# Kernel optimization log

Hardware: AMD Instinct MI355X
Metric: run time of the kernel (lower is better)

Reference implementation:

```python
import math
import jax, jax.numpy as jnp
import numpy as np

NUM_HEADS = 12
HEAD_DIM = 64
HIDDEN = NUM_HEADS * HEAD_DIM  # 768
SEQ = 4096


def setup_inputs() -> dict:
    key = jax.random.key(0)
    ks = jax.random.split(key, 7)
    s = 0.02  # BERT-style init scale for weights
    return {
        "hidden_states": jax.random.normal(ks[0], (1, SEQ, HIDDEN), jnp.float32),
        "Wq": jax.random.normal(ks[1], (HIDDEN, HIDDEN), jnp.float32) * s,
        "bq": jax.random.normal(ks[2], (HIDDEN,), jnp.float32) * s,
        "Wk": jax.random.normal(ks[3], (HIDDEN, HIDDEN), jnp.float32) * s,
        "bk": jax.random.normal(ks[4], (HIDDEN,), jnp.float32) * s,
        "Wv": jax.random.normal(ks[5], (HIDDEN, HIDDEN), jnp.float32) * s,
        "bv": jax.random.normal(ks[6], (HIDDEN,), jnp.float32) * s,
    }


def _split_heads(z):
    # [S, HIDDEN] -> [H, S, dh]
    S = z.shape[0]
    return jnp.transpose(z.reshape(S, NUM_HEADS, HEAD_DIM), (1, 0, 2))


def reference(hidden_states, Wq, bq, Wk, bk, Wv, bv):
    # batch is squeezed in the original module (kernel is unbatched)
    x = hidden_states[0]  # [S, D]
    q = _split_heads(x @ Wq.T + bq)  # [H, S, dh]
    k = _split_heads(x @ Wk.T + bk)  # [H, S, dh]
    scale = 1.0 / math.sqrt(HEAD_DIM)
    scores = jnp.einsum('hqd,hkd->hqk', q, k) * scale  # [H, S, S]
    probs = jax.nn.softmax(scores, axis=-1)
    # multi_rand_attn_cuda approximates P @ (x @ Wv^T + bv) via CDF-driven
    # Monte-Carlo column sampling of Wv; its expectation is the exact product,
    # which is the correctness baseline computed here.
    v = _split_heads(x @ Wv.T + bv)  # [H, S, dh]
    ctx = jnp.einsum('hqk,hkd->hqd', probs, v)  # [H, S, dh]
    ctx = jnp.transpose(ctx, (1, 0, 2)).reshape(x.shape[0], HIDDEN)
    return ctx[None]  # [1, S, D]
```

## Files before the change

kernel.cpp:

```cpp
#include <hip/hip_runtime.h>
#include <stdint.h>


typedef float    f32x4 __attribute__((ext_vector_type(4)));
typedef _Float16 h16x8 __attribute__((ext_vector_type(8)));
typedef _Float16 h16x4 __attribute__((ext_vector_type(4)));
typedef _Float16 h16x2 __attribute__((ext_vector_type(2)));
typedef __fp16   fp16x2 __attribute__((ext_vector_type(2)));
typedef unsigned short u16;

#define MFMA32(A, B, C) __builtin_amdgcn_mfma_f32_16x16x32_f16((A), (B), (C), 0, 0, 0)
#define ZERO4 ((f32x4){0.f, 0.f, 0.f, 0.f})

#define SEQ 4096
#define HID 768
#define NH  12
#define DH  64

#define CEXP 0.18033688011112042f

#define WAITV(N) asm volatile("s_waitcnt vmcnt(" #N ")" ::: "memory")
#define SBAR()   __builtin_amdgcn_s_barrier()
#define SCHED0() __builtin_amdgcn_sched_barrier(0)

__device__ __forceinline__ u16 f2h(float f) {
  union { _Float16 h; u16 u; } v;
  v.h = (_Float16)f;
  return v.u;
}
__device__ __forceinline__ float h2f(u16 u) {
  union { u16 u; _Float16 h; } v;
  v.u = u;
  return (float)v.h;
}

__device__ __forceinline__ void gload_lds16(const void* g, void* l) {
  __builtin_amdgcn_global_load_lds(
      (__attribute__((address_space(1))) void*)(g),
      (__attribute__((address_space(3))) void*)(l),
      16, 0, 0);
}

__global__ __launch_bounds__(256) void cast_all_k(
    const float* __restrict__ x,  const float* __restrict__ wq,
    const float* __restrict__ wk, const float* __restrict__ wv,
    u16* __restrict__ xh,  u16* __restrict__ wqh,
    u16* __restrict__ wkh, u16* __restrict__ wvh)
{
  int i = blockIdx.x * 256 + threadIdx.x;
  const int NX4 = (SEQ * HID) / 4;
  const int NW4 = (HID * HID) / 4;
  const float4* src; ushort4* dst; int idx;
  if (i < NX4) {
    src = (const float4*)x; dst = (ushort4*)xh; idx = i;
  } else {
    int j = i - NX4;
    int w = j / NW4;
    idx = j - w * NW4;
    src = (const float4*)(w == 0 ? wq : (w == 1 ? wk : wv));
    dst = (ushort4*)(w == 0 ? wqh : (w == 1 ? wkh : wvh));
  }
  float4 v = src[idx];
  ushort4 o;
  o.x = f2h(v.x); o.y = f2h(v.y); o.z = f2h(v.z); o.w = f2h(v.w);
  dst[idx] = o;
}

__global__ __launch_bounds__(256, 3) void qkv_gemm_k(
    const u16* __restrict__ xh,
    const u16* __restrict__ wqh, const u16* __restrict__ wkh, const u16* __restrict__ wvh,
    const float* __restrict__ bq, const float* __restrict__ bk, const float* __restrict__ bv,
    u16* __restrict__ Qh, u16* __restrict__ Kh, u16* __restrict__ Vt)
{
  __shared__ u16 S[128 * 128];

  const int t = threadIdx.x;
  const int wave = t >> 6, lane = t & 63;
  const int m = lane & 15, quad = lane >> 4;
  const int z  = blockIdx.z;
  const int n0 = blockIdx.x * 128;
  const int m0 = blockIdx.y * 128;

  const u16*   W    = (z == 0) ? wqh : (z == 1) ? wkh : wvh;
  const float* bias = (z == 0) ? bq  : (z == 1) ? bk  : bv;

  const int wm = (wave >> 1) * 64;
  const int wn = (wave & 1) * 64;

  f32x4 acc[4][4];
#pragma unroll
  for (int i = 0; i < 4; i++)
#pragma unroll
    for (int j = 0; j < 4; j++) acc[i][j] = ZERO4;

  const int srow = wave * 8 + (lane >> 3);
  const int scg  = (lane & 7) ^ (srow & 7);
  const u16* gA = xh + (m0 + srow) * HID + scg * 8;
  const u16* gB = W  + (n0 + srow) * HID + scg * 8;
  u16* lA = S + wave * 512;
  u16* lB = S + 8192 + wave * 512;

  for (int k0 = 0; k0 < HID; k0 += 64) {
    __syncthreads();
#pragma unroll
    for (int c = 0; c < 4; c++) {
      gload_lds16(gA + c * 32 * HID + k0, lA + c * 2048);
      gload_lds16(gB + c * 32 * HID + k0, lB + c * 2048);
    }
    __syncthreads();

#pragma unroll
    for (int s = 0; s < 2; s++) {
      h16x8 af[4], bf[4];
#pragma unroll
      for (int i = 0; i < 4; i++)
        af[i] = *(const h16x8*)(S + (wm + i * 16 + m) * 64
                                + ((s * 4 + quad) ^ (m & 7)) * 8);
#pragma unroll
      for (int j = 0; j < 4; j++)
        bf[j] = *(const h16x8*)(S + 8192 + (wn + j * 16 + m) * 64
                                + ((s * 4 + quad) ^ (m & 7)) * 8);
#pragma unroll
      for (int i = 0; i < 4; i++)
#pragma unroll
        for (int j = 0; j < 4; j++)
          acc[i][j] = MFMA32(af[i], bf[j], acc[i][j]);
    }
  }

  __syncthreads();

  if (z < 2) {
    const float sc = (z == 0) ? CEXP : 1.0f;
#pragma unroll
    for (int i = 0; i < 4; i++) {
      int sl = wm + i * 16 + quad * 4;
#pragma unroll
      for (int j = 0; j < 4; j++) {
        int colp = wn + j * 16 + m;
        float bb = bias[n0 + colp];
        int c = colp >> 3, sub = colp & 7;
#pragma unroll
        for (int r = 0; r < 4; r++)
          S[(sl + r) * 128 + ((c ^ ((sl + r) & 15)) * 8) + sub] =
              f2h((acc[i][j][r] + bb) * sc);
      }
    }
    __syncthreads();
    u16* outp = (z == 0) ? Qh : Kh;
    const int ch = t & 15;
#pragma unroll
    for (int rr = 0; rr < 8; rr++) {
      int s = rr * 16 + (t >> 4);
      h16x8 v = *(const h16x8*)(S + s * 128 + ((ch ^ (s & 15)) * 8));
      *(h16x8*)(outp + (m0 + s) * HID + n0 + ch * 8) = v;
    }
  } else {
#pragma unroll
    for (int i = 0; i < 4; i++) {
      int sl = wm + i * 16 + quad * 4;
      int vp = (sl & ~31) + ((sl >> 2) & 3) * 8 + ((sl >> 4) & 1) * 4;
#pragma unroll
      for (int j = 0; j < 4; j++) {
        int nl = wn + j * 16 + m;
        float bb = bias[n0 + nl];
        h16x4 o;
        o[0] = (_Float16)(acc[i][j][0] + bb);
        o[1] = (_Float16)(acc[i][j][1] + bb);
        o[2] = (_Float16)(acc[i][j][2] + bb);
        o[3] = (_Float16)(acc[i][j][3] + bb);
        *(h16x4*)(S + nl * 128 + (((vp >> 3) ^ (nl & 15)) * 8) + (vp & 7)) = o;
      }
    }
    __syncthreads();
    const int ch = t & 15;
#pragma unroll
    for (int rr = 0; rr < 8; rr++) {
      int n = rr * 16 + (t >> 4);
      h16x8 v = *(const h16x8*)(S + n * 128 + ((ch ^ (n & 15)) * 8));
      *(h16x8*)(Vt + (n0 + n) * SEQ + m0 + ch * 8) = v;
    }
  }
}


__device__ __forceinline__ void stage_kv(const u16* gKb, const u16* gVb,
                                         u16* lK, u16* lV, int kv0)
{
#pragma unroll
  for (int c = 0; c < 2; c++) {
    gload_lds16(gKb + (kv0 + c * 32) * HID, lK + c * 2048);
    gload_lds16(gVb + c * 32 * SEQ + kv0,   lV + c * 2048);
  }
}

__device__ __forceinline__ void attn_compute(
    const u16* __restrict__ Kb, const u16* __restrict__ Vb,
    const h16x8 (&qf)[2][2], f32x4 (&O)[2][4], f32x4 (&Lacc)[2],
    h16x8 onesv, int m, int quad)
{
#pragma unroll
  for (int p = 0; p < 2; ++p) {
    const int krow0 = 32 * p + m;
    const int krow1 = krow0 + 16;
    h16x8 kb00 = *(const h16x8*)(Kb + krow0 * 64 + ((    quad) ^ (m & 7)) * 8);
    h16x8 kb01 = *(const h16x8*)(Kb + krow0 * 64 + ((4 + quad) ^ (m & 7)) * 8);
    h16x8 kb10 = *(const h16x8*)(Kb + krow1 * 64 + ((    quad) ^ (m & 7)) * 8);
    h16x8 kb11 = *(const h16x8*)(Kb + krow1 * 64 + ((4 + quad) ^ (m & 7)) * 8);

    h16x8 vb[4];
#pragma unroll
    for (int jd = 0; jd < 4; jd++) {
      int d = jd * 16 + m;
      vb[jd] = *(const h16x8*)(Vb + d * 64 + (((p * 4 + quad) ^ (m & 7)) * 8));
    }

#pragma unroll
    for (int qn = 0; qn < 2; qn++) {
      __builtin_amdgcn_s_setprio(1);
      f32x4 S0 = MFMA32(kb00, qf[qn][0], ZERO4);
      S0       = MFMA32(kb01, qf[qn][1], S0);
      f32x4 S1 = MFMA32(kb10, qf[qn][0], ZERO4);
      S1       = MFMA32(kb11, qf[qn][1], S1);
      __builtin_amdgcn_s_setprio(0);

      float e0 = __builtin_amdgcn_exp2f(S0[0]);
      float e1 = __builtin_amdgcn_exp2f(S0[1]);
      float e2 = __builtin_amdgcn_exp2f(S0[2]);
      float e3 = __builtin_amdgcn_exp2f(S0[3]);
      float e4 = __builtin_amdgcn_exp2f(S1[0]);
      float e5 = __builtin_amdgcn_exp2f(S1[1]);
      float e6 = __builtin_amdgcn_exp2f(S1[2]);
      float e7 = __builtin_amdgcn_exp2f(S1[3]);

      fp16x2 p01 = __builtin_amdgcn_cvt_pkrtz(e0, e1);
      fp16x2 p23 = __builtin_amdgcn_cvt_pkrtz(e2, e3);
      fp16x2 p45 = __builtin_amdgcn_cvt_pkrtz(e4, e5);
      fp16x2 p67 = __builtin_amdgcn_cvt_pkrtz(e6, e7);
      h16x2 q01 = __builtin_bit_cast(h16x2, p01);
      h16x2 q23 = __builtin_bit_cast(h16x2, p23);
      h16x2 q45 = __builtin_bit_cast(h16x2, p45);
      h16x2 q67 = __builtin_bit_cast(h16x2, p67);
      h16x4 pl = __builtin_shufflevector(q01, q23, 0, 1, 2, 3);
      h16x4 ph = __builtin_shufflevector(q45, q67, 0, 1, 2, 3);
      h16x8 pa = __builtin_shufflevector(pl, ph, 0, 1, 2, 3, 4, 5, 6, 7);

      __builtin_amdgcn_s_setprio(1);
#pragma unroll
      for (int jd = 0; jd < 4; jd++)
        O[qn][jd] = MFMA32(pa, vb[jd], O[qn][jd]);
      Lacc[qn] = MFMA32(pa, onesv, Lacc[qn]);
      __builtin_amdgcn_s_setprio(0);
    }
  }
}

__global__ __launch_bounds__(256, 3) void attn_k(
    const u16* __restrict__ Qh, const u16* __restrict__ Kh, const u16* __restrict__ Vt,
    float* __restrict__ out0, u16* __restrict__ Op1, float* __restrict__ Lp)
{
  __shared__ u16 Ks[3][64 * 64];
  __shared__ u16 Vs[3][64 * 64];

  const int t = threadIdx.x;
  const int wave = t >> 6, lane = t & 63;
  const int m = lane & 15, quad = lane >> 4;
  const int h  = blockIdx.y;
  const int q0 = blockIdx.x * 128;
  const int sp = blockIdx.z;
  const int kvbase = sp * 2048;

  h16x8 qf[2][2];
#pragma unroll
  for (int qn = 0; qn < 2; qn++)
#pragma unroll
    for (int ks = 0; ks < 2; ks++)
      qf[qn][ks] = *(const h16x8*)(Qh + (q0 + wave * 32 + qn * 16 + m) * HID
                                   + h * DH + ks * 32 + quad * 8);

  f32x4 O[2][4];
#pragma unroll
  for (int qn = 0; qn < 2; qn++)
#pragma unroll
    for (int jd = 0; jd < 4; jd++) O[qn][jd] = ZERO4;
  f32x4 Lacc[2] = {ZERO4, ZERO4};

  h16x8 onesv;
#pragma unroll
  for (int j = 0; j < 8; j++) onesv[j] = (_Float16)1.0f;

  const int srow = wave * 8 + (lane >> 3);
  const int swz  = ((lane & 7) ^ (srow & 7)) * 8;
  const u16* gKb = Kh + srow * HID + h * DH + swz;
  const u16* gVb = Vt + (h * DH + srow) * SEQ + swz;
  u16* lK0 = &Ks[0][wave * 512]; u16* lV0 = &Vs[0][wave * 512];
  u16* lK1 = &Ks[1][wave * 512]; u16* lV1 = &Vs[1][wave * 512];
  u16* lK2 = &Ks[2][wave * 512]; u16* lV2 = &Vs[2][wave * 512];

  stage_kv(gKb, gVb, lK0, lV0, kvbase);
  stage_kv(gKb, gVb, lK1, lV1, kvbase + 64);

  for (int it = 0; it < 30; it += 3) {
    WAITV(4); SBAR(); SCHED0();
    stage_kv(gKb, gVb, lK2, lV2, kvbase + (it + 2) * 64);
    attn_compute(&Ks[0][0], &Vs[0][0], qf, O, Lacc, onesv, m, quad);
    SCHED0();

    WAITV(4); SBAR(); SCHED0();
    stage_kv(gKb, gVb, lK0, lV0, kvbase + (it + 3) * 64);
    attn_compute(&Ks[1][0], &Vs[1][0], qf, O, Lacc, onesv, m, quad);
    SCHED0();

    WAITV(4); SBAR(); SCHED0();
    stage_kv(gKb, gVb, lK1, lV1, kvbase + (it + 4) * 64);
    attn_compute(&Ks[2][0], &Vs[2][0], qf, O, Lacc, onesv, m, quad);
    SCHED0();
  }
  WAITV(4); SBAR(); SCHED0();
  attn_compute(&Ks[0][0], &Vs[0][0], qf, O, Lacc, onesv, m, quad);
  SCHED0();
  WAITV(0); SBAR(); SCHED0();
  attn_compute(&Ks[1][0], &Vs[1][0], qf, O, Lacc, onesv, m, quad);

#pragma unroll
  for (int qn = 0; qn < 2; qn++) {
    if (m == 0) {
#pragma unroll
      for (int r = 0; r < 4; r++)
        Lp[sp * NH * SEQ + h * SEQ + q0 + wave * 32 + qn * 16 + quad * 4 + r] =
            Lacc[qn][r];
    }
#pragma unroll
    for (int jd = 0; jd < 4; jd++) {
      int col = h * DH + jd * 16 + m;
#pragma unroll
      for (int r = 0; r < 4; r++) {
        int row = q0 + wave * 32 + qn * 16 + quad * 4 + r;
        if (sp == 0) out0[row * HID + col] = O[qn][jd][r];
        else         Op1[row * HID + col] = f2h(O[qn][jd][r]);
      }
    }
  }
}

__global__ __launch_bounds__(256) void reduce_k(
    float* __restrict__ out, const u16* __restrict__ Op1,
    const float* __restrict__ Lp)
{
  int i = blockIdx.x * 256 + threadIdx.x;
  int s  = i / 192;
  int c4 = i - s * 192;
  int h  = c4 >> 4;
  float L = Lp[h * SEQ + s] + Lp[NH * SEQ + h * SEQ + s];
  float inv = __builtin_amdgcn_rcpf(L);
  float4 a = ((const float4*)out)[i];
  ushort4 b = ((const ushort4*)Op1)[i];
  float4 r;
  r.x = (a.x + h2f(b.x)) * inv;
  r.y = (a.y + h2f(b.y)) * inv;
  r.z = (a.z + h2f(b.z)) * inv;
  r.w = (a.w + h2f(b.w)) * inv;
  ((float4*)out)[i] = r;
}

extern "C" void kernel_launch(void* const* d_in, const int* in_sizes, int n_in,
                              void* d_out, int out_size, void* d_ws, size_t ws_size,
                              hipStream_t stream) {
  const float* x  = (const float*)d_in[0];
  const float* Wq = (const float*)d_in[1];
  const float* bq = (const float*)d_in[2];
  const float* Wk = (const float*)d_in[3];
  const float* bk = (const float*)d_in[4];
  const float* Wv = (const float*)d_in[5];
  const float* bv = (const float*)d_in[6];
  float* out = (float*)d_out;

  char* ws = (char*)d_ws;
  u16* Qh  = (u16*)(ws);
  u16* Kh  = (u16*)(ws + 6291456);
  u16* Vt  = (u16*)(ws + 12582912);
  u16* xh  = (u16*)(ws + 18874368);
  u16* wqh = (u16*)(ws + 25165824);
  u16* wkh = (u16*)(ws + 26345472);
  u16* wvh = (u16*)(ws + 27525120);
  u16*   Op1 = (u16*)(ws + 18874368);
  float* Lp  = (float*)(ws + 25165824);

  cast_all_k<<<4800, 256, 0, stream>>>(x, Wq, Wk, Wv, xh, wqh, wkh, wvh);
  qkv_gemm_k<<<dim3(6, 32, 3), 256, 0, stream>>>(xh, wqh, wkh, wvh,
                                                 bq, bk, bv, Qh, Kh, Vt);
  attn_k<<<dim3(32, NH, 2), 256, 0, stream>>>(Qh, Kh, Vt, out, Op1, Lp);
  reduce_k<<<3072, 256, 0, stream>>>(out, Op1, Lp);
}
```

Measured before the change: 158.1 us.

## Load K tiles directly into double-buffered registers instead of staging in LDS

K tiles for the attention loop are now read straight from global memory into two alternating register banks, one tile ahead of use. V alone is staged through LDS, now in a four-slot ring. The wait counts are rewritten to match the new load order. This removes the LDS round trip and LDS traffic for K, but every wave now fetches the full K tile itself, which multiplies K global/L2 reads, and it adds 64 VGPRs of register pressure under a 3-block occupancy bound.

```diff
diff --git a/kernel.cpp b/kernel.cpp
--- a/kernel.cpp
+++ b/kernel.cpp
@@ -184,30 +184,34 @@
 }
 
 
-__device__ __forceinline__ void stage_kv(const u16* gKb, const u16* gVb,
-                                         u16* lK, u16* lV, int kv0)
-{
-#pragma unroll
-  for (int c = 0; c < 2; c++) {
-    gload_lds16(gKb + (kv0 + c * 32) * HID, lK + c * 2048);
-    gload_lds16(gVb + c * 32 * SEQ + kv0,   lV + c * 2048);
-  }
+__device__ __forceinline__ void stage_v(const u16* gVb, u16* lV, int kv0)
+{
+#pragma unroll
+  for (int c = 0; c < 2; c++)
+    gload_lds16(gVb + c * 32 * SEQ + kv0, lV + c * 2048);
+}
+
+__device__ __forceinline__ void prefK(const u16* kt, int vo0, int vo1,
+                                      h16x8 (&bank)[8])
+{
+  const u16* kt2 = kt + 32 * HID;
+  bank[0] = *(const h16x8*)(kt  + vo0);
+  bank[1] = *(const h16x8*)(kt  + vo0 + 32);
+  bank[2] = *(const h16x8*)(kt  + vo1);
+  bank[3] = *(const h16x8*)(kt  + vo1 + 32);
+  bank[4] = *(const h16x8*)(kt2 + vo0);
+  bank[5] = *(const h16x8*)(kt2 + vo0 + 32);
+  bank[6] = *(const h16x8*)(kt2 + vo1);
+  bank[7] = *(const h16x8*)(kt2 + vo1 + 32);
 }
 
 __device__ __forceinline__ void attn_compute(
-    const u16* __restrict__ Kb, const u16* __restrict__ Vb,
+    const h16x8 (&kb)[8], const u16* __restrict__ Vb,
     const h16x8 (&qf)[2][2], f32x4 (&O)[2][4], f32x4 (&Lacc)[2],
     h16x8 onesv, int m, int quad)
 {
 #pragma unroll
   for (int p = 0; p < 2; ++p) {
-    const int krow0 = 32 * p + m;
-    const int krow1 = krow0 + 16;
-    h16x8 kb00 = *(const h16x8*)(Kb + krow0 * 64 + ((    quad) ^ (m & 7)) * 8);
-    h16x8 kb01 = *(const h16x8*)(Kb + krow0 * 64 + ((4 + quad) ^ (m & 7)) * 8);
-    h16x8 kb10 = *(const h16x8*)(Kb + krow1 * 64 + ((    quad) ^ (m & 7)) * 8);
-    h16x8 kb11 = *(const h16x8*)(Kb + krow1 * 64 + ((4 + quad) ^ (m & 7)) * 8);
-
     h16x8 vb[4];
 #pragma unroll
     for (int jd = 0; jd < 4; jd++) {
@@ -218,10 +222,10 @@
 #pragma unroll
     for (int qn = 0; qn < 2; qn++) {
       __builtin_amdgcn_s_setprio(1);
-      f32x4 S0 = MFMA32(kb00, qf[qn][0], ZERO4);
-      S0       = MFMA32(kb01, qf[qn][1], S0);
-      f32x4 S1 = MFMA32(kb10, qf[qn][0], ZERO4);
-      S1       = MFMA32(kb11, qf[qn][1], S1);
+      f32x4 S0 = MFMA32(kb[p * 4 + 0], qf[qn][0], ZERO4);
+      S0       = MFMA32(kb[p * 4 + 1], qf[qn][1], S0);
+      f32x4 S1 = MFMA32(kb[p * 4 + 2], qf[qn][0], ZERO4);
+      S1       = MFMA32(kb[p * 4 + 3], qf[qn][1], S1);
       __builtin_amdgcn_s_setprio(0);
 
       float e0 = __builtin_amdgcn_exp2f(S0[0]);
@@ -255,12 +259,21 @@
   }
 }
 
+#define ABODY(T, BKC, BKP, DO_PREF, DO_STAGE, WN)                           \
+  WAITV(WN); SBAR(); SCHED0();                                              \
+  if (DO_PREF) { prefK(ktp, vo0, vo1, BKP); ktp += 64 * HID; }              \
+  SCHED0();                                                                 \
+  if (DO_STAGE) stage_v(gVb, &Vs[(T + 2) & 3][wave * 512],                  \
+                        kvbase + ((T) + 2) * 64);                           \
+  SCHED0();                                                                 \
+  attn_compute(BKC, &Vs[(T) & 3][0], qf, O, Lacc, onesv, m, quad);          \
+  SCHED0();
+
 __global__ __launch_bounds__(256, 3) void attn_k(
     const u16* __restrict__ Qh, const u16* __restrict__ Kh, const u16* __restrict__ Vt,
     float* __restrict__ out0, u16* __restrict__ Op1, float* __restrict__ Lp)
 {
-  __shared__ u16 Ks[3][64 * 64];
-  __shared__ u16 Vs[3][64 * 64];
+  __shared__ u16 Vs[4][64 * 64];
 
   const int t = threadIdx.x;
   const int wave = t >> 6, lane = t & 63;
@@ -291,36 +304,31 @@
 
   const int srow = wave * 8 + (lane >> 3);
   const int swz  = ((lane & 7) ^ (srow & 7)) * 8;
-  const u16* gKb = Kh + srow * HID + h * DH + swz;
   const u16* gVb = Vt + (h * DH + srow) * SEQ + swz;
-  u16* lK0 = &Ks[0][wave * 512]; u16* lV0 = &Vs[0][wave * 512];
-  u16* lK1 = &Ks[1][wave * 512]; u16* lV1 = &Vs[1][wave * 512];
-  u16* lK2 = &Ks[2][wave * 512]; u16* lV2 = &Vs[2][wave * 512];
-
-  stage_kv(gKb, gVb, lK0, lV0, kvbase);
-  stage_kv(gKb, gVb, lK1, lV1, kvbase + 64);
-
-  for (int it = 0; it < 30; it += 3) {
-    WAITV(4); SBAR(); SCHED0();
-    stage_kv(gKb, gVb, lK2, lV2, kvbase + (it + 2) * 64);
-    attn_compute(&Ks[0][0], &Vs[0][0], qf, O, Lacc, onesv, m, quad);
-    SCHED0();
-
-    WAITV(4); SBAR(); SCHED0();
-    stage_kv(gKb, gVb, lK0, lV0, kvbase + (it + 3) * 64);
-    attn_compute(&Ks[1][0], &Vs[1][0], qf, O, Lacc, onesv, m, quad);
-    SCHED0();
-
-    WAITV(4); SBAR(); SCHED0();
-    stage_kv(gKb, gVb, lK1, lV1, kvbase + (it + 4) * 64);
-    attn_compute(&Ks[2][0], &Vs[2][0], qf, O, Lacc, onesv, m, quad);
-    SCHED0();
-  }
-  WAITV(4); SBAR(); SCHED0();
-  attn_compute(&Ks[0][0], &Vs[0][0], qf, O, Lacc, onesv, m, quad);
+
+  const int vo0 = m * HID + quad * 8;
+  const int vo1 = vo0 + 16 * HID;
+  const u16* ktp = Kh + h * DH + kvbase * HID;
+
+  h16x8 bkA[8], bkB[8];
+
+  stage_v(gVb, &Vs[0][wave * 512], kvbase);
   SCHED0();
-  WAITV(0); SBAR(); SCHED0();
-  attn_compute(&Ks[1][0], &Vs[1][0], qf, O, Lacc, onesv, m, quad);
+  prefK(ktp, vo0, vo1, bkA); ktp += 64 * HID;
+  SCHED0();
+  stage_v(gVb, &Vs[1][wave * 512], kvbase + 64);
+  SCHED0();
+
+  for (int it = 0; it < 28; it += 4) {
+    ABODY(it + 0, bkA, bkB, 1, 1, 2)
+    ABODY(it + 1, bkB, bkA, 1, 1, 2)
+    ABODY(it + 2, bkA, bkB, 1, 1, 2)
+    ABODY(it + 3, bkB, bkA, 1, 1, 2)
+  }
+  ABODY(28, bkA, bkB, 1, 1, 2)
+  ABODY(29, bkB, bkA, 1, 1, 2)
+  ABODY(30, bkA, bkB, 1, 0, 2)
+  ABODY(31, bkB, bkA, 0, 0, 0)
 
 #pragma unroll
   for (int qn = 0; qn < 2; qn++) {
```

Measured after the change: 204.4 us. +29.2%, slower.

## Triple-buffer QKV GEMM LDS staging with async prefetch pipeline

Applied to the files above, without the earlier changes.

Restructures the QKV projection GEMM main loop from a synchronous load-then-compute scheme with K-step 64 into a three-stage ring of LDS buffers with K-step 32. Global-to-LDS loads for step k+2 are issued before computing step k, and vmcnt waits plus a single barrier per step replace the two __syncthreads per iteration. The MFMA burst is wrapped in s_setprio to favour matrix issue. LDS use rises to 48KB, which may limit occupancy to 3 blocks per CU, and the shorter K step doubles the number of barriers.

```diff
diff --git a/kernel.cpp b/kernel.cpp
--- a/kernel.cpp
+++ b/kernel.cpp
@@ -66,13 +66,45 @@
   dst[idx] = o;
 }
 
+
+__device__ __forceinline__ void qstage(const u16* gA, const u16* gB,
+                                       u16* buf, int wave, int k0)
+{
+#pragma unroll
+  for (int c = 0; c < 2; c++) {
+    gload_lds16(gA + c * 64 * HID + k0, buf + c * 2048 + wave * 512);
+    gload_lds16(gB + c * 64 * HID + k0, buf + 4096 + c * 2048 + wave * 512);
+  }
+}
+
+__device__ __forceinline__ void qcompute(const u16* buf, f32x4 (&acc)[4][4],
+                                         int wm, int wn, int m, int quad)
+{
+  h16x8 af[4], bf[4];
+  const int cs = (quad ^ (m & 3)) * 8;
+#pragma unroll
+  for (int i = 0; i < 4; i++)
+    af[i] = *(const h16x8*)(buf + (wm + i * 16 + m) * 32 + cs);
+#pragma unroll
+  for (int j = 0; j < 4; j++)
+    bf[j] = *(const h16x8*)(buf + 4096 + (wn + j * 16 + m) * 32 + cs);
+  __builtin_amdgcn_s_setprio(1);
+#pragma unroll
+  for (int i = 0; i < 4; i++)
+#pragma unroll
+    for (int j = 0; j < 4; j++)
+      acc[i][j] = MFMA32(af[i], bf[j], acc[i][j]);
+  __builtin_amdgcn_s_setprio(0);
+}
+
 __global__ __launch_bounds__(256, 3) void qkv_gemm_k(
     const u16* __restrict__ xh,
     const u16* __restrict__ wqh, const u16* __restrict__ wkh, const u16* __restrict__ wvh,
     const float* __restrict__ bq, const float* __restrict__ bk, const float* __restrict__ bv,
     u16* __restrict__ Qh, u16* __restrict__ Kh, u16* __restrict__ Vt)
 {
-  __shared__ u16 S[128 * 128];
+  __shared__ u16 S[3][8192];
+  u16* Sf = &S[0][0];
 
   const int t = threadIdx.x;
   const int wave = t >> 6, lane = t & 63;
@@ -93,40 +125,34 @@
 #pragma unroll
     for (int j = 0; j < 4; j++) acc[i][j] = ZERO4;
 
-  const int srow = wave * 8 + (lane >> 3);
-  const int scg  = (lane & 7) ^ (srow & 7);
+  const int srow = wave * 16 + (lane >> 2);
+  const int scg  = (lane & 3) ^ (srow & 3);
   const u16* gA = xh + (m0 + srow) * HID + scg * 8;
   const u16* gB = W  + (n0 + srow) * HID + scg * 8;
-  u16* lA = S + wave * 512;
-  u16* lB = S + 8192 + wave * 512;
-
-  for (int k0 = 0; k0 < HID; k0 += 64) {
-    __syncthreads();
-#pragma unroll
-    for (int c = 0; c < 4; c++) {
-      gload_lds16(gA + c * 32 * HID + k0, lA + c * 2048);
-      gload_lds16(gB + c * 32 * HID + k0, lB + c * 2048);
-    }
-    __syncthreads();
-
-#pragma unroll
-    for (int s = 0; s < 2; s++) {
-      h16x8 af[4], bf[4];
-#pragma unroll
-      for (int i = 0; i < 4; i++)
-        af[i] = *(const h16x8*)(S + (wm + i * 16 + m) * 64
-                                + ((s * 4 + quad) ^ (m & 7)) * 8);
-#pragma unroll
-      for (int j = 0; j < 4; j++)
-        bf[j] = *(const h16x8*)(S + 8192 + (wn + j * 16 + m) * 64
-                                + ((s * 4 + quad) ^ (m & 7)) * 8);
-#pragma unroll
-      for (int i = 0; i < 4; i++)
-#pragma unroll
-        for (int j = 0; j < 4; j++)
-          acc[i][j] = MFMA32(af[i], bf[j], acc[i][j]);
-    }
-  }
+
+  qstage(gA, gB, &S[0][0], wave, 0);
+  qstage(gA, gB, &S[1][0], wave, 32);
+
+  for (int it = 0; it < 21; it += 3) {
+    WAITV(4); SBAR(); SCHED0();
+    qstage(gA, gB, &S[2][0], wave, (it + 2) * 32);
+    qcompute(&S[0][0], acc, wm, wn, m, quad); SCHED0();
+
+    WAITV(4); SBAR(); SCHED0();
+    qstage(gA, gB, &S[0][0], wave, (it + 3) * 32);
+    qcompute(&S[1][0], acc, wm, wn, m, quad); SCHED0();
+
+    WAITV(4); SBAR(); SCHED0();
+    qstage(gA, gB, &S[1][0], wave, (it + 4) * 32);
+    qcompute(&S[2][0], acc, wm, wn, m, quad); SCHED0();
+  }
+  WAITV(4); SBAR(); SCHED0();
+  qstage(gA, gB, &S[2][0], wave, 23 * 32);
+  qcompute(&S[0][0], acc, wm, wn, m, quad); SCHED0();
+  WAITV(4); SBAR(); SCHED0();
+  qcompute(&S[1][0], acc, wm, wn, m, quad); SCHED0();
+  WAITV(0); SBAR(); SCHED0();
+  qcompute(&S[2][0], acc, wm, wn, m, quad); SCHED0();
 
   __syncthreads();
 
@@ -142,7 +168,7 @@
         int c = colp >> 3, sub = colp & 7;
 #pragma unroll
         for (int r = 0; r < 4; r++)
-          S[(sl + r) * 128 + ((c ^ ((sl + r) & 15)) * 8) + sub] =
+          Sf[(sl + r) * 128 + ((c ^ ((sl + r) & 15)) * 8) + sub] =
               f2h((acc[i][j][r] + bb) * sc);
       }
     }
@@ -152,7 +178,7 @@
 #pragma unroll
     for (int rr = 0; rr < 8; rr++) {
       int s = rr * 16 + (t >> 4);
-      h16x8 v = *(const h16x8*)(S + s * 128 + ((ch ^ (s & 15)) * 8));
+      h16x8 v = *(const h16x8*)(Sf + s * 128 + ((ch ^ (s & 15)) * 8));
       *(h16x8*)(outp + (m0 + s) * HID + n0 + ch * 8) = v;
     }
   } else {
@@ -169,7 +195,7 @@
         o[1] = (_Float16)(acc[i][j][1] + bb);
         o[2] = (_Float16)(acc[i][j][2] + bb);
         o[3] = (_Float16)(acc[i][j][3] + bb);
-        *(h16x4*)(S + nl * 128 + (((vp >> 3) ^ (nl & 15)) * 8) + (vp & 7)) = o;
+        *(h16x4*)(Sf + nl * 128 + (((vp >> 3) ^ (nl & 15)) * 8) + (vp & 7)) = o;
       }
     }
     __syncthreads();
@@ -177,7 +203,7 @@
 #pragma unroll
     for (int rr = 0; rr < 8; rr++) {
       int n = rr * 16 + (t >> 4);
-      h16x8 v = *(const h16x8*)(S + n * 128 + ((ch ^ (n & 15)) * 8));
+      h16x8 v = *(const h16x8*)(Sf + n * 128 + ((ch ^ (n & 15)) * 8));
       *(h16x8*)(Vt + (n0 + n) * SEQ + m0 + ch * 8) = v;
     }
   }
```

Measured after the change: 165.4 us. 1.05x slower.
